# Optimization experiments

Hardware: AMD Instinct MI355X
Metric: run time of the kernel (lower is better)

The kernel has to match this reference:

```python
import jax, jax.numpy as jnp
import numpy as np

DIM = 512; LAYERS = 6; K = 15; VOCAB = 32000; B = 2; L = 1024
HID = 1024  # SwiGLU hidden: int(512*2) rounded up to multiple of 64
RANK = 64; BLOCK = 2048; MIX_W = 0.1
UP_DIL = [1, 2, 4, 8, 16, 32]
DN_DIL = UP_DIL[::-1]


def rmsnorm(x, w, eps=1e-6):
    return x * jax.lax.rsqrt(jnp.mean(x * x, axis=-1, keepdims=True) + eps) * w


def dconv(x, w, b, dil):
    # x: [B,D,T]; w: [D,1,K] depthwise; left (causal) padding of (K-1)*dil
    pad = (w.shape[-1] - 1) * dil
    y = jax.lax.conv_general_dilated(
        x, w, window_strides=(1,), padding=[(pad, 0)], rhs_dilation=(dil,),
        dimension_numbers=('NCH', 'OIH', 'NCH'), feature_group_count=x.shape[1])
    return y + b[None, :, None]


def conv_block(x, nw, cw, cb, w1, w2, w3, dil):
    # CausalDilatedConv: RMSNorm -> depthwise causal dilated conv -> silu -> SwiGLU -> +residual
    h = rmsnorm(x, nw)
    h = jax.nn.silu(dconv(jnp.transpose(h, (0, 2, 1)), cw, cb, dil))
    h = jnp.transpose(h, (0, 2, 1))
    h = jnp.einsum('bth,dh->btd',
                   jax.nn.silu(jnp.einsum('btd,hd->bth', h, w1)) * jnp.einsum('btd,hd->bth', h, w3),
                   w2)
    return h + x


def run_stack(x, dils, nw, cw, cb, w1, w2, w3, kp, ki, kd, gnorm):
    integral = x; previous = x; current = x
    for i, d in enumerate(dils):
        if i > 0:
            # PIDGate: step == i >= 1 so max(step,1) == i
            pid = kp[i-1] * current + ki[i-1] * (integral / i) + kd[i-1] * (current - previous)
            cur_in = rmsnorm(jax.nn.silu(pid), gnorm[i-1])
        else:
            cur_in = current
        current = conv_block(cur_in, nw[i], cw[i], cb[i], w1[i], w2[i], w3[i], d)
        previous = current
        integral = integral + current
    return current


def mix(x):
    # CausalMeanPool: x + 0.1 * causal running mean
    counts = jnp.arange(1, x.shape[1] + 1, dtype=x.dtype)[None, :, None]
    return x + MIX_W * jnp.cumsum(x, axis=1) / counts


def sgate(new, old, nw, dw, db, uw, ub):
    h = jax.nn.silu(rmsnorm(new, nw) @ dw.T + db)
    g = jax.nn.sigmoid(h @ uw.T + ub)
    return g * new + (1.0 - g) * old


def setup_inputs() -> dict:
    key = jax.random.key(0)
    ks = iter(jax.random.split(key, 64))
    def nrm(shape, s=0.02):
        return jax.random.normal(next(ks), shape, jnp.float32) * s
    def stack_params(p):
        return {
            p + '_norm_w': jnp.ones((LAYERS, DIM), jnp.float32),
            p + '_conv_w': nrm((LAYERS, DIM, 1, K), 0.1),
            p + '_conv_b': jnp.zeros((LAYERS, DIM), jnp.float32),
            p + '_w1': nrm((LAYERS, HID, DIM)),
            p + '_w2': nrm((LAYERS, DIM, HID)),
            p + '_w3': nrm((LAYERS, HID, DIM)),
            p + '_kp': jnp.full((LAYERS - 1, DIM), 0.5, jnp.float32),
            p + '_ki': jnp.full((LAYERS - 1, DIM), 0.3, jnp.float32),
            p + '_kd': jnp.full((LAYERS - 1, DIM), 0.2, jnp.float32),
            p + '_gnorm': jnp.ones((LAYERS - 1, DIM), jnp.float32),
        }
    inp = {
        'idx': jax.random.randint(next(ks), (B, L), 0, VOCAB),
        'emb': nrm((VOCAB, DIM)),
        'pos': nrm((1, BLOCK, DIM)),
        'emb_norm_w': jnp.ones((DIM,), jnp.float32),
        'token_shift': jnp.full((DIM,), 0.5, jnp.float32),
        'mem_gate_w': jnp.zeros((DIM, DIM), jnp.float32),  # nn.init.zeros_
        'mem_gate_b': nrm((DIM,)),
        'memory_p': jnp.zeros((B, DIM), jnp.float32),  # buffer, zero after reset()
        'sg_norm': jnp.ones((3, DIM), jnp.float32),
        'sg_down_w': nrm((3, RANK, DIM)),
        'sg_down_b': jnp.zeros((3, RANK), jnp.float32),
        'sg_up_w': nrm((3, DIM, RANK)),
        'sg_up_b': jnp.zeros((3, DIM), jnp.float32),
        'final_norm_w': jnp.ones((DIM,), jnp.float32),
    }
    inp.update(stack_params('up'))
    inp.update(stack_params('dn'))
    return inp


def _forward(idx, emb, pos, emb_norm_w, token_shift, mem_gate_w, mem_gate_b, memory_p,
             up_norm_w, up_conv_w, up_conv_b, up_w1, up_w2, up_w3, up_kp, up_ki, up_kd, up_gnorm,
             dn_norm_w, dn_conv_w, dn_conv_b, dn_w1, dn_w2, dn_w3, dn_kp, dn_ki, dn_kd, dn_gnorm,
             sg_norm, sg_down_w, sg_down_b, sg_up_w, sg_up_b, final_norm_w):
    T = idx.shape[1]
    x = emb[idx] + pos[:, :T]
    x = rmsnorm(x, emb_norm_w)
    # dropout is identity at eval time
    # memory injection: token-shift mix + sigmoid-gated persistent P-memory
    shifted = jnp.concatenate(
        [x[:, :1], token_shift * x[:, :-1] + (1.0 - token_shift) * x[:, 1:]], axis=1)
    mem = jax.nn.sigmoid(memory_p @ mem_gate_w.T + mem_gate_b)
    x = shifted + mem[:, None, :]
    initial = x
    up_p = (up_norm_w, up_conv_w, up_conv_b, up_w1, up_w2, up_w3, up_kp, up_ki, up_kd, up_gnorm)
    dn_p = (dn_norm_w, dn_conv_w, dn_conv_b, dn_w1, dn_w2, dn_w3, dn_kp, dn_ki, dn_kd, dn_gnorm)
    up1 = mix(run_stack(x, UP_DIL, *up_p))
    gated1 = sgate(up1, initial, sg_norm[0], sg_down_w[0], sg_down_b[0], sg_up_w[0], sg_up_b[0])
    down = mix(run_stack(gated1, DN_DIL, *dn_p))
    gated2 = sgate(down, initial, sg_norm[1], sg_down_w[1], sg_down_b[1], sg_up_w[1], sg_up_b[1])
    up2 = mix(run_stack(gated2, UP_DIL, *up_p))  # up_stack weights are shared/reused
    output = sgate(up2, gated2, sg_norm[2], sg_down_w[2], sg_down_b[2], sg_up_w[2], sg_up_b[2])
    output = rmsnorm(output, final_norm_w)
    return output @ emb.T  # tied head


def reference(idx, emb, pos, emb_norm_w, token_shift, mem_gate_w, mem_gate_b, memory_p,
              up_norm_w, up_conv_w, up_conv_b, up_w1, up_w2, up_w3, up_kp, up_ki, up_kd, up_gnorm,
              dn_norm_w, dn_conv_w, dn_conv_b, dn_w1, dn_w2, dn_w3, dn_kp, dn_ki, dn_kd, dn_gnorm,
              sg_norm, sg_down_w, sg_down_b, sg_up_w, sg_up_b, final_norm_w):
    return _forward(idx, emb, pos, emb_norm_w, token_shift, mem_gate_w, mem_gate_b, memory_p,
                    up_norm_w, up_conv_w, up_conv_b, up_w1, up_w2, up_w3, up_kp, up_ki, up_kd, up_gnorm,
                    dn_norm_w, dn_conv_w, dn_conv_b, dn_w1, dn_w2, dn_w3, dn_kp, dn_ki, dn_kd, dn_gnorm,
                    sg_norm, sg_down_w, sg_down_b, sg_up_w, sg_up_b, final_norm_w)
```

## Files before the change

### kernel.cpp

```cpp
#include <hip/hip_runtime.h>
#include <math.h>

#define DIM 512
#define NLAYERS 6
#define KSZ 15
#define VOCAB 32000
#define BATCH 2
#define SEQ 1024
#define HIDN 1024
#define RANK 64
#define NTOK (BATCH*SEQ)
#define MIXW 0.1f

typedef unsigned short u16;
typedef _Float16 f16;
typedef _Float16 f16x8 __attribute__((ext_vector_type(8)));
typedef _Float16 f16x4 __attribute__((ext_vector_type(4)));
typedef float  f32x4  __attribute__((ext_vector_type(4)));

__device__ __forceinline__ float sigm(float x){ return 1.f/(1.f+__expf(-x)); }

__device__ __forceinline__ float wred(float v){
  #pragma unroll
  for (int o=32;o>0;o>>=1) v += __shfl_xor(v, o, 64);
  return v;
}

#define MFMA16(a,b,c) __builtin_amdgcn_mfma_f32_16x16x32_f16(a,b,c,0,0,0)

__device__ __forceinline__ void gld16(const f16* g, f16* l){
  __builtin_amdgcn_global_load_lds(
      (const __attribute__((address_space(1))) void*)g,
      (__attribute__((address_space(3))) void*)l, 16, 0, 0);
}

__global__ __launch_bounds__(256) void k_cvt(const float* __restrict__ s,
    f16* __restrict__ d, long n4){
  long i = (long)blockIdx.x*256 + threadIdx.x;
  if (i >= n4) return;
  float4 v = reinterpret_cast<const float4*>(s)[i];
  f16x4 o; o.x=(f16)v.x; o.y=(f16)v.y; o.z=(f16)v.z; o.w=(f16)v.w;
  reinterpret_cast<f16x4*>(d)[i] = o;
}

__global__ __launch_bounds__(256) void k_cvtconv(const float* __restrict__ cw,
    float* __restrict__ cwT, int n){
  int i = blockIdx.x*256 + threadIdx.x;
  if (i >= n) return;
  int d = i & (DIM-1); int m = (i >> 9) % KSZ; int l = i / (KSZ*DIM);
  cwT[i] = cw[((size_t)l*DIM + d)*KSZ + (KSZ-1-m)];
}

__global__ __launch_bounds__(64) void k_embnorm(const int* __restrict__ idx,
    const float* __restrict__ emb, const float* __restrict__ pos,
    const float* __restrict__ w, float* __restrict__ out){
  int row = blockIdx.x;
  int t = row & (SEQ-1);
  int lane = threadIdx.x;
  long ebase = (long)idx[row]*DIM;
  long pbase = (long)t*DIM;
  float v[8]; float ss = 0.f;
  #pragma unroll
  for (int c=0;c<2;c++){
    int d = c*256 + lane*4;
    float4 e = *reinterpret_cast<const float4*>(emb + ebase + d);
    float4 p = *reinterpret_cast<const float4*>(pos + pbase + d);
    float x0 = e.x+p.x, x1 = e.y+p.y, x2 = e.z+p.z, x3 = e.w+p.w;
    v[c*4+0]=x0; v[c*4+1]=x1; v[c*4+2]=x2; v[c*4+3]=x3;
    ss += x0*x0 + x1*x1 + x2*x2 + x3*x3;
  }
  ss = wred(ss);
  float rs = rsqrtf(ss*(1.f/DIM) + 1e-6f);
  long ob = (long)row*DIM;
  #pragma unroll
  for (int c=0;c<2;c++){
    int d = c*256 + lane*4;
    float4 wv = *reinterpret_cast<const float4*>(w + d);
    float4 o;
    o.x = v[c*4+0]*rs*wv.x; o.y = v[c*4+1]*rs*wv.y;
    o.z = v[c*4+2]*rs*wv.z; o.w = v[c*4+3]*rs*wv.w;
    *reinterpret_cast<float4*>(out + ob + d) = o;
  }
}

__global__ void k_mem(const float* __restrict__ p, const float* __restrict__ gw,
                      const float* __restrict__ gb, float* __restrict__ mem){
  int i = blockIdx.x*blockDim.x + threadIdx.x;
  if (i >= BATCH*DIM) return;
  int b = i >> 9, d = i & (DIM-1);
  float acc = gb[d];
  const float* wr = gw + (long)d*DIM;
  const float* pr = p + b*DIM;
  for (int k=0;k<DIM;k+=4){
    float4 wv = *reinterpret_cast<const float4*>(wr+k);
    float4 pv = *reinterpret_cast<const float4*>(pr+k);
    acc += wv.x*pv.x + wv.y*pv.y + wv.z*pv.z + wv.w*pv.w;
  }
  mem[i] = sigm(acc);
}

__global__ void k_shift(const float* __restrict__ xn, const float* __restrict__ mem,
    const float* __restrict__ ts, float* __restrict__ out){
  int i = blockIdx.x*256 + threadIdx.x;
  int d = i & (DIM-1); int row = i >> 9; int t = row & (SEQ-1); int b = row >> 10;
  float cur = xn[i];
  float v;
  if (t == 0) v = cur;
  else { float f = ts[d]; v = f*xn[i-DIM] + (1.f-f)*cur; }
  out[i] = v + mem[b*DIM + d];
}

__global__ __launch_bounds__(64) void k_rms(const float* __restrict__ x,
    const float* __restrict__ w, f16* __restrict__ oh){
  int row = blockIdx.x; int lane = threadIdx.x;
  const float* xr = x + (long)row*DIM;
  float v[8]; float ss = 0.f;
  #pragma unroll
  for (int c=0;c<2;c++){
    int d = c*256 + lane*4;
    float4 f = *reinterpret_cast<const float4*>(xr + d);
    v[c*4+0]=f.x; v[c*4+1]=f.y; v[c*4+2]=f.z; v[c*4+3]=f.w;
    ss += f.x*f.x + f.y*f.y + f.z*f.z + f.w*f.w;
  }
  ss = wred(ss);
  float rs = rsqrtf(ss*(1.f/DIM) + 1e-6f);
  long ob = (long)row*DIM;
  #pragma unroll
  for (int c=0;c<2;c++){
    int d = c*256 + lane*4;
    float4 wv = *reinterpret_cast<const float4*>(w + d);
    f16x4 o;
    o.x = (f16)(v[c*4+0]*rs*wv.x); o.y = (f16)(v[c*4+1]*rs*wv.y);
    o.z = (f16)(v[c*4+2]*rs*wv.z); o.w = (f16)(v[c*4+3]*rs*wv.w);
    *reinterpret_cast<f16x4*>(oh + ob + d) = o;
  }
}

__global__ __launch_bounds__(64) void k_pid(const float* __restrict__ C,
    const float* __restrict__ I, float inv_i,
    const float* __restrict__ kp, const float* __restrict__ ki,
    const float* __restrict__ gn, const float* __restrict__ nw,
    float* __restrict__ xin, f16* __restrict__ oh){
  int row = blockIdx.x; int lane = threadIdx.x;
  long base = (long)row*DIM;
  float u[8]; float ss = 0.f;
  #pragma unroll
  for (int c=0;c<2;c++){
    int d = c*256 + lane*4;
    float4 cv = *reinterpret_cast<const float4*>(C + base + d);
    float4 iv = *reinterpret_cast<const float4*>(I + base + d);
    float4 kpv = *reinterpret_cast<const float4*>(kp + d);
    float4 kiv = *reinterpret_cast<const float4*>(ki + d);
    float p0 = kpv.x*cv.x + kiv.x*(iv.x*inv_i);
    float p1 = kpv.y*cv.y + kiv.y*(iv.y*inv_i);
    float p2 = kpv.z*cv.z + kiv.z*(iv.z*inv_i);
    float p3 = kpv.w*cv.w + kiv.w*(iv.w*inv_i);
    float s0 = p0*sigm(p0), s1 = p1*sigm(p1), s2 = p2*sigm(p2), s3 = p3*sigm(p3);
    u[c*4+0]=s0; u[c*4+1]=s1; u[c*4+2]=s2; u[c*4+3]=s3;
    ss += s0*s0 + s1*s1 + s2*s2 + s3*s3;
  }
  ss = wred(ss);
  float rs1 = rsqrtf(ss*(1.f/DIM) + 1e-6f);
  float x2[8]; float ss2 = 0.f;
  #pragma unroll
  for (int c=0;c<2;c++){
    int d = c*256 + lane*4;
    float4 gv = *reinterpret_cast<const float4*>(gn + d);
    float y0 = u[c*4+0]*rs1*gv.x, y1 = u[c*4+1]*rs1*gv.y;
    float y2 = u[c*4+2]*rs1*gv.z, y3 = u[c*4+3]*rs1*gv.w;
    x2[c*4+0]=y0; x2[c*4+1]=y1; x2[c*4+2]=y2; x2[c*4+3]=y3;
    ss2 += y0*y0 + y1*y1 + y2*y2 + y3*y3;
    float4 o; o.x=y0; o.y=y1; o.z=y2; o.w=y3;
    *reinterpret_cast<float4*>(xin + base + d) = o;
  }
  ss2 = wred(ss2);
  float rs2 = rsqrtf(ss2*(1.f/DIM) + 1e-6f);
  #pragma unroll
  for (int c=0;c<2;c++){
    int d = c*256 + lane*4;
    float4 nv = *reinterpret_cast<const float4*>(nw + d);
    f16x4 o;
    o.x = (f16)(x2[c*4+0]*rs2*nv.x); o.y = (f16)(x2[c*4+1]*rs2*nv.y);
    o.z = (f16)(x2[c*4+2]*rs2*nv.z); o.w = (f16)(x2[c*4+3]*rs2*nv.w);
    *reinterpret_cast<f16x4*>(oh + base + d) = o;
  }
}

__global__ __launch_bounds__(256) void k_conv(const f16* __restrict__ h1,
    const float* __restrict__ cwT, const float* __restrict__ cb,
    f16* __restrict__ hc, int dil){
  int i = blockIdx.x*256 + threadIdx.x;
  int d8 = (i & 63) << 3; int row = i >> 6; int t = row & (SEQ-1);
  float acc[8];
  {
    float4 b0 = *reinterpret_cast<const float4*>(&cb[d8]);
    float4 b1 = *reinterpret_cast<const float4*>(&cb[d8+4]);
    acc[0]=b0.x; acc[1]=b0.y; acc[2]=b0.z; acc[3]=b0.w;
    acc[4]=b1.x; acc[5]=b1.y; acc[6]=b1.z; acc[7]=b1.w;
  }
  #pragma unroll
  for (int m=0;m<KSZ;m++){
    if (t - m*dil >= 0){
      f16x8 h = *reinterpret_cast<const f16x8*>(&h1[(size_t)(row - m*dil)*DIM + d8]);
      float4 w0 = *reinterpret_cast<const float4*>(&cwT[m*DIM + d8]);
      float4 w1 = *reinterpret_cast<const float4*>(&cwT[m*DIM + d8 + 4]);
      acc[0]+=w0.x*(float)h[0]; acc[1]+=w0.y*(float)h[1];
      acc[2]+=w0.z*(float)h[2]; acc[3]+=w0.w*(float)h[3];
      acc[4]+=w1.x*(float)h[4]; acc[5]+=w1.y*(float)h[5];
      acc[6]+=w1.z*(float)h[6]; acc[7]+=w1.w*(float)h[7];
    }
  }
  f16x8 o;
  #pragma unroll
  for (int j=0;j<8;j++){ o[j] = (f16)(acc[j]*sigm(acc[j])); }
  *reinterpret_cast<f16x8*>(&hc[(size_t)row*DIM + d8]) = o;
}


__global__ __launch_bounds__(512) void k_dual(const f16* __restrict__ A,
    const f16* __restrict__ W1, const f16* __restrict__ W3, f16* __restrict__ G){
  __shared__ __align__(16) char smemc[50176];
  f16*   sB   = (f16*)smemc;
  float* stgf = (float*)smemc;
  float* kred = (float*)smemc + 4352;
  int tid = threadIdx.x, lane = tid&63, wid = tid>>6;
  int wk = wid>>2, wm = wid&3;
  int m0 = blockIdx.x*128, n0 = blockIdx.y*64;
  int r16 = lane&15, kq = lane>>4;

  auto stage = [&](int buf, int t){
    #pragma unroll
    for (int j=0;j<2;j++){
      int cc = j*512 + tid;
      int mat = cc>>9, c2 = cc&511, r = c2>>3, s = c2&7;
      const f16* src = (mat ? W3 : W1) + (size_t)(n0+r)*512 + t*64 + ((s^(r&7))<<3);
      gld16(src, sB + buf*8192 + (j*512 + wid*64)*8);
    }
  };

  f32x4 acc[2][4] = {};
  stage(0, 0);
  __syncthreads();
  #pragma unroll
  for (int t=0;t<8;t++){
    if (t < 7) stage((t&1)^1, t+1);
    f16x8 af[2][2];
    #pragma unroll
    for (int kk=0;kk<2;kk++)
      #pragma unroll
      for (int mf=0;mf<2;mf++){
        int row = m0 + wm*32 + mf*16 + r16;
        af[kk][mf] = *reinterpret_cast<const f16x8*>(A + (size_t)row*512 + t*64 + (kk*4+kq)*8);
      }
    const f16* sbt = sB + (t&1)*8192 + wk*4096;
    #pragma unroll
    for (int kk=0;kk<2;kk++){
      int kp0 = kk*4 + kq;
      f16x8 bf[4];
      #pragma unroll
      for (int nf=0;nf<4;nf++){
        int row = nf*16 + r16;
        bf[nf] = *reinterpret_cast<const f16x8*>(&sbt[row*64 + ((kp0^(row&7))<<3)]);
      }
      #pragma unroll
      for (int mf=0;mf<2;mf++)
        #pragma unroll
        for (int nf=0;nf<4;nf++)
          acc[mf][nf] = MFMA16(af[kk][mf], bf[nf], acc[mf][nf]);
    }
    __syncthreads();
  }
  if (wk == 1){
    #pragma unroll
    for (int mf=0;mf<2;mf++)
      #pragma unroll
      for (int nf=0;nf<4;nf++)
        *reinterpret_cast<f32x4*>(&kred[(((wm*2+mf)*4+nf)<<8) + lane*4]) = acc[mf][nf];
  }
  __syncthreads();
  if (wk == 1) return;
  int dr = (lane>>4)*4, dc = lane&15;
  float* stg = stgf + wm*1088;
  #pragma unroll
  for (int mf=0;mf<2;mf++){
    #pragma unroll
    for (int nf=0;nf<4;nf++){
      f32x4 a3 = *reinterpret_cast<f32x4*>(&kred[(((wm*2+mf)*4+nf)<<8) + lane*4]);
      #pragma unroll
      for (int q=0;q<4;q++){
        float x1 = acc[mf][nf][q];
        stg[(dr+q)*68 + nf*16 + dc] = x1*sigm(x1)*a3[q];
      }
    }
    int gmb = m0 + wm*32 + mf*16;
    #pragma unroll
    for (int pass=0;pass<2;pass++){
      int rr = pass*8 + (lane>>3), c = 8*(lane&7);
      float4 lo = *reinterpret_cast<float4*>(&stg[rr*68 + c]);
      float4 hi = *reinterpret_cast<float4*>(&stg[rr*68 + c + 4]);
      f16x8 o;
      o[0]=(f16)lo.x; o[1]=(f16)lo.y; o[2]=(f16)lo.z; o[3]=(f16)lo.w;
      o[4]=(f16)hi.x; o[5]=(f16)hi.y; o[6]=(f16)hi.z; o[7]=(f16)hi.w;
      *reinterpret_cast<f16x8*>(&G[(size_t)(gmb+rr)*HIDN + n0 + c]) = o;
    }
  }
}

__global__ __launch_bounds__(512) void k_w2(const f16* __restrict__ A,
    const f16* __restrict__ W, const float* __restrict__ XIN,
    float* __restrict__ OF, float* __restrict__ I, int init){
  __shared__ __align__(16) char smemc[33792];
  f16*   sB   = (f16*)smemc;
  float* stgf = (float*)smemc;
  float* kred = (float*)smemc + 4352;
  int tid = threadIdx.x, lane = tid&63, wid = tid>>6;
  int wk = wid>>2, wm = wid&3;
  int m0 = blockIdx.x*64, n0 = blockIdx.y*64;
  int r16 = lane&15, kq = lane>>4;

  auto stage = [&](int buf, int t){
    #pragma unroll
    for (int j=0;j<2;j++){
      int cc = j*512 + tid;
      int kg = cc>>9, c2 = cc&511, r = c2>>3, s = c2&7;
      const f16* src = W + (size_t)(n0+r)*1024 + kg*512 + t*64 + ((s^(r&7))<<3);
      gld16(src, sB + buf*8192 + (j*512 + wid*64)*8);
    }
  };

  f32x4 acc[4] = {};
  stage(0, 0);
  __syncthreads();
  #pragma unroll
  for (int t=0;t<8;t++){
    if (t < 7) stage((t&1)^1, t+1);
    f16x8 af[2];
    #pragma unroll
    for (int kk=0;kk<2;kk++){
      int row = m0 + wm*16 + r16;
      af[kk] = *reinterpret_cast<const f16x8*>(A + (size_t)row*1024 + wk*512 + t*64 + (kk*4+kq)*8);
    }
    const f16* sbt = sB + (t&1)*8192 + wk*4096;
    #pragma unroll
    for (int kk=0;kk<2;kk++){
      int kp0 = kk*4 + kq;
      #pragma unroll
      for (int nf=0;nf<4;nf++){
        int row = nf*16 + r16;
        f16x8 bf = *reinterpret_cast<const f16x8*>(&sbt[row*64 + ((kp0^(row&7))<<3)]);
        acc[nf] = MFMA16(af[kk], bf, acc[nf]);
      }
    }
    __syncthreads();
  }
  if (wk == 1){
    #pragma unroll
    for (int nf=0;nf<4;nf++)
      *reinterpret_cast<f32x4*>(&kred[((wm*4+nf)<<8) + lane*4]) = acc[nf];
  }
  __syncthreads();
  if (wk == 1) return;
  #pragma unroll
  for (int nf=0;nf<4;nf++){
    f32x4 p = *reinterpret_cast<f32x4*>(&kred[((wm*4+nf)<<8) + lane*4]);
    acc[nf][0]+=p[0]; acc[nf][1]+=p[1]; acc[nf][2]+=p[2]; acc[nf][3]+=p[3];
  }
  int dr = (lane>>4)*4, dc = lane&15;
  float* stg = stgf + wm*1088;
  #pragma unroll
  for (int nf=0;nf<4;nf++)
    #pragma unroll
    for (int q=0;q<4;q++)
      stg[(dr+q)*68 + nf*16 + dc] = acc[nf][q];
  int gmb = m0 + wm*16;
  #pragma unroll
  for (int pass=0;pass<4;pass++){
    int rr = pass*4 + (lane>>4), c = 4*(lane&15);
    float4 v = *reinterpret_cast<float4*>(&stg[rr*68 + c]);
    size_t o = (size_t)(gmb+rr)*DIM + n0 + c;
    float4 x = *reinterpret_cast<const float4*>(&XIN[o]);
    v.x+=x.x; v.y+=x.y; v.z+=x.z; v.w+=x.w;
    *reinterpret_cast<float4*>(&OF[o]) = v;
    float4 iv;
    if (init) iv = x;
    else      iv = *reinterpret_cast<const float4*>(&I[o]);
    iv.x+=v.x; iv.y+=v.y; iv.z+=v.z; iv.w+=v.w;
    *reinterpret_cast<float4*>(&I[o]) = iv;
  }
}

__global__ __launch_bounds__(512) void k_logits(const f16* __restrict__ A,
    const f16* __restrict__ E, float* __restrict__ OF){
  __shared__ __align__(16) char smemc[34816];
  f16*   sB   = (f16*)smemc;
  float* stgf = (float*)smemc;
  int tid = threadIdx.x, lane = tid&63, wid = tid>>6;
  int bid = blockIdx.x;
  int m0 = (bid&7)*256, n0 = (bid>>3)*64;
  int r16 = lane&15, kq = lane>>4;

  auto stage = [&](int buf, int t){
    int cc = tid;
    int r = cc>>3, s = cc&7;
    const f16* src = E + (size_t)(n0+r)*512 + t*64 + ((s^(r&7))<<3);
    gld16(src, sB + buf*4096 + wid*64*8);
  };

  f32x4 acc[2][4] = {};
  stage(0, 0);
  __syncthreads();
  #pragma unroll
  for (int t=0;t<8;t++){
    if (t < 7) stage((t&1)^1, t+1);
    f16x8 af[2][2];
    #pragma unroll
    for (int kk=0;kk<2;kk++)
      #pragma unroll
      for (int mf=0;mf<2;mf++){
        int row = m0 + wid*32 + mf*16 + r16;
        af[kk][mf] = *reinterpret_cast<const f16x8*>(A + (size_t)row*512 + t*64 + (kk*4+kq)*8);
      }
    const f16* sbt = sB + (t&1)*4096;
    #pragma unroll
    for (int kk=0;kk<2;kk++){
      int kp0 = kk*4 + kq;
      f16x8 bf[4];
      #pragma unroll
      for (int nf=0;nf<4;nf++){
        int row = nf*16 + r16;
        bf[nf] = *reinterpret_cast<const f16x8*>(&sbt[row*64 + ((kp0^(row&7))<<3)]);
      }
      #pragma unroll
      for (int mf=0;mf<2;mf++)
        #pragma unroll
        for (int nf=0;nf<4;nf++)
          acc[mf][nf] = MFMA16(af[kk][mf], bf[nf], acc[mf][nf]);
    }
    __syncthreads();
  }
  int dr = (lane>>4)*4, dc = lane&15;
  float* stg = stgf + wid*1088;
  #pragma unroll
  for (int mf=0;mf<2;mf++){
    #pragma unroll
    for (int nf=0;nf<4;nf++)
      #pragma unroll
      for (int q=0;q<4;q++)
        stg[(dr+q)*68 + nf*16 + dc] = acc[mf][nf][q];
    int gmb = m0 + wid*32 + mf*16;
    #pragma unroll
    for (int pass=0;pass<4;pass++){
      int rr = pass*4 + (lane>>4), c = 4*(lane&15);
      float4 v = *reinterpret_cast<float4*>(&stg[rr*68 + c]);
      *reinterpret_cast<float4*>(&OF[(size_t)(gmb+rr)*VOCAB + n0 + c]) = v;
    }
  }
}

__global__ __launch_bounds__(64) void k_mix(float* __restrict__ x){
  int col = blockIdx.x;
  int b = col >> 9, d = col & (DIM-1);
  int lane = threadIdx.x;
  long o = (long)b*SEQ*DIM + d + (long)lane*16*DIM;
  float v[16]; float s = 0.f;
  #pragma unroll
  for (int j=0;j<16;j++){ v[j] = x[o + (long)j*DIM]; s += v[j]; }
  float t = s;
  #pragma unroll
  for (int off=1; off<64; off<<=1){
    float u = __shfl_up(t, off, 64);
    if (lane >= off) t += u;
  }
  float run = t - s;
  #pragma unroll
  for (int j=0;j<16;j++){
    run += v[j];
    int tt = lane*16 + j;
    x[o + (long)j*DIM] = v[j] + MIXW*run/(float)(tt+1);
  }
}

__global__ __launch_bounds__(256) void k_sgate(const float* __restrict__ xnew,
    const float* __restrict__ xold, const float* __restrict__ nw,
    const float* __restrict__ dw, const float* __restrict__ db,
    const float* __restrict__ uw, const float* __restrict__ ub,
    float* __restrict__ out){
  __shared__ float raw[DIM];
  __shared__ float xn[DIM];
  __shared__ float part[256];
  __shared__ float hb[RANK];
  int row = blockIdx.x, tid = threadIdx.x;
  long base = (long)row*DIM;
  float ss = 0.f;
  for (int d=tid; d<DIM; d+=256){ float v = xnew[base+d]; raw[d]=v; ss += v*v; }
  ss = wred(ss);
  if ((tid&63)==0) part[tid>>6] = ss;
  __syncthreads();
  float tot = part[0]+part[1]+part[2]+part[3];
  float rs = rsqrtf(tot*(1.f/DIM)+1e-6f);
  for (int d=tid; d<DIM; d+=256) xn[d] = raw[d]*rs*nw[d];
  __syncthreads();
  int rr = tid & 63, q = tid >> 6;
  float p = 0.f;
  const float* dwr = dw + (long)rr*DIM + q*128;
  const float* xq = xn + q*128;
  #pragma unroll 8
  for (int d=0; d<128; d+=4){
    float4 wv = *reinterpret_cast<const float4*>(dwr+d);
    p += xq[d]*wv.x + xq[d+1]*wv.y + xq[d+2]*wv.z + xq[d+3]*wv.w;
  }
  part[tid] = p;
  __syncthreads();
  if (tid < RANK){
    float h = part[tid] + part[64+tid] + part[128+tid] + part[192+tid] + db[tid];
    hb[tid] = h * sigm(h);
  }
  __syncthreads();
  for (int d=tid; d<DIM; d+=256){
    float a = ub[d];
    const float* ur = uw + (long)d*RANK;
    #pragma unroll
    for (int rj=0;rj<RANK;rj+=4){
      float4 uv = *reinterpret_cast<const float4*>(ur+rj);
      a += hb[rj]*uv.x + hb[rj+1]*uv.y + hb[rj+2]*uv.z + hb[rj+3]*uv.w;
    }
    float g = sigm(a);
    out[base+d] = g*raw[d] + (1.f-g)*xold[base+d];
  }
}

extern "C" void kernel_launch(void* const* d_in, const int* in_sizes, int n_in,
                              void* d_out, int out_size, void* d_ws, size_t ws_size,
                              hipStream_t stream){
  const int*   idx           = (const int*)d_in[0];
  const float* emb           = (const float*)d_in[1];
  const float* pos           = (const float*)d_in[2];
  const float* emb_norm_w    = (const float*)d_in[3];
  const float* token_shift   = (const float*)d_in[4];
  const float* mem_gate_w    = (const float*)d_in[5];
  const float* mem_gate_b    = (const float*)d_in[6];
  const float* memory_p      = (const float*)d_in[7];
  const float* sg_norm       = (const float*)d_in[8];
  const float* sg_down_w     = (const float*)d_in[9];
  const float* sg_down_b     = (const float*)d_in[10];
  const float* sg_up_w       = (const float*)d_in[11];
  const float* sg_up_b       = (const float*)d_in[12];
  const float* final_norm_w  = (const float*)d_in[13];
  struct StackP { const float *nw, *cw, *cb, *w1, *w2, *w3, *kp, *ki, *gn; };
  StackP up { (const float*)d_in[14], (const float*)d_in[15], (const float*)d_in[16],
              (const float*)d_in[17], (const float*)d_in[18], (const float*)d_in[19],
              (const float*)d_in[20], (const float*)d_in[21], (const float*)d_in[23] };
  StackP dn { (const float*)d_in[24], (const float*)d_in[25], (const float*)d_in[26],
              (const float*)d_in[27], (const float*)d_in[28], (const float*)d_in[29],
              (const float*)d_in[30], (const float*)d_in[31], (const float*)d_in[33] };

  char* wp = (char*)d_ws;
  auto alloc = [&](size_t bytes)->void*{
    void* p = (void*)wp; wp += (bytes + 255) & ~(size_t)255; return p;
  };
  float* A0  = (float*)alloc((size_t)NTOK*DIM*4);
  float* A1  = (float*)alloc((size_t)NTOK*DIM*4);
  float* Cb  = (float*)alloc((size_t)NTOK*DIM*4);
  float* Ib  = (float*)alloc((size_t)NTOK*DIM*4);
  float* XIN = (float*)alloc((size_t)NTOK*DIM*4);
  f16*   H1  = (f16*)alloc((size_t)NTOK*DIM*2);
  f16*   HC  = (f16*)alloc((size_t)NTOK*DIM*2);
  f16*   G   = (f16*)alloc((size_t)NTOK*HIDN*2);
  const size_t WSZ = (size_t)NLAYERS*HIDN*DIM;
  f16*   UpW1 = (f16*)alloc(WSZ*2);
  f16*   UpW2 = (f16*)alloc(WSZ*2);
  f16*   UpW3 = (f16*)alloc(WSZ*2);
  f16*   DnW1 = (f16*)alloc(WSZ*2);
  f16*   DnW2 = (f16*)alloc(WSZ*2);
  f16*   DnW3 = (f16*)alloc(WSZ*2);
  f16*   Ef   = (f16*)alloc((size_t)VOCAB*DIM*2);
  float* UpCT = (float*)alloc((size_t)NLAYERS*KSZ*DIM*4);
  float* DnCT = (float*)alloc((size_t)NLAYERS*KSZ*DIM*4);
  float* MEM  = (float*)alloc((size_t)BATCH*DIM*4);

  static const int updil[NLAYERS] = {1,2,4,8,16,32};
  static const int dndil[NLAYERS] = {32,16,8,4,2,1};

  {
    long n4 = WSZ/4;
    int g = (int)((n4 + 255)/256);
    k_cvt<<<g,256,0,stream>>>(up.w1, UpW1, n4);
    k_cvt<<<g,256,0,stream>>>(up.w2, UpW2, n4);
    k_cvt<<<g,256,0,stream>>>(up.w3, UpW3, n4);
    k_cvt<<<g,256,0,stream>>>(dn.w1, DnW1, n4);
    k_cvt<<<g,256,0,stream>>>(dn.w2, DnW2, n4);
    k_cvt<<<g,256,0,stream>>>(dn.w3, DnW3, n4);
    long e4 = (long)VOCAB*DIM/4;
    k_cvt<<<(int)((e4+255)/256),256,0,stream>>>(emb, Ef, e4);
    int nc = NLAYERS*KSZ*DIM;
    k_cvtconv<<<(nc+255)/256,256,0,stream>>>(up.cw, UpCT, nc);
    k_cvtconv<<<(nc+255)/256,256,0,stream>>>(dn.cw, DnCT, nc);
  }

  k_embnorm<<<NTOK,64,0,stream>>>(idx, emb, pos, emb_norm_w, Cb);
  k_mem<<<(BATCH*DIM+255)/256,256,0,stream>>>(memory_p, mem_gate_w, mem_gate_b, MEM);
  k_shift<<<NTOK*DIM/256,256,0,stream>>>(Cb, MEM, token_shift, A0);

  auto run_stack = [&](const float* xs, const StackP& S, const float* CT,
                       const f16* W1f, const f16* W2f, const f16* W3f, const int* dil){
    for (int l=0;l<NLAYERS;l++){
      const float* bin;
      if (l==0){
        bin = xs;
        k_rms<<<NTOK,64,0,stream>>>(xs, S.nw + l*DIM, H1);
      } else {
        k_pid<<<NTOK,64,0,stream>>>(Cb, Ib, 1.f/(float)l,
            S.kp+(l-1)*DIM, S.ki+(l-1)*DIM, S.gn+(l-1)*DIM, S.nw+l*DIM, XIN, H1);
        bin = XIN;
      }
      k_conv<<<NTOK*DIM/8/256,256,0,stream>>>(H1, CT + (size_t)l*KSZ*DIM, S.cb + l*DIM, HC, dil[l]);
      k_dual<<<dim3(NTOK/128, HIDN/64),512,0,stream>>>(
          HC, W1f + (size_t)l*HIDN*DIM, W3f + (size_t)l*HIDN*DIM, G);
      k_w2<<<dim3(NTOK/64, DIM/64),512,0,stream>>>(
          G, W2f + (size_t)l*DIM*HIDN, bin, Cb, Ib, (l==0)?1:0);
    }
  };

  run_stack(A0, up, UpCT, UpW1, UpW2, UpW3, updil);
  k_mix<<<BATCH*DIM,64,0,stream>>>(Cb);
  k_sgate<<<NTOK,256,0,stream>>>(Cb, A0, sg_norm, sg_down_w, sg_down_b, sg_up_w, sg_up_b, A1);
  run_stack(A1, dn, DnCT, DnW1, DnW2, DnW3, dndil);
  k_mix<<<BATCH*DIM,64,0,stream>>>(Cb);
  k_sgate<<<NTOK,256,0,stream>>>(Cb, A0, sg_norm+DIM, sg_down_w+RANK*DIM, sg_down_b+RANK,
                                 sg_up_w+DIM*RANK, sg_up_b+DIM, A1);
  run_stack(A1, up, UpCT, UpW1, UpW2, UpW3, updil);
  k_mix<<<BATCH*DIM,64,0,stream>>>(Cb);
  k_sgate<<<NTOK,256,0,stream>>>(Cb, A1, sg_norm+2*DIM, sg_down_w+2*RANK*DIM, sg_down_b+2*RANK,
                                 sg_up_w+2*DIM*RANK, sg_up_b+2*DIM, Cb);
  k_rms<<<NTOK,64,0,stream>>>(Cb, final_norm_w, H1);
  k_logits<<<8*(VOCAB/64),512,0,stream>>>(H1, Ef, (float*)d_out);
}
```

Measured before the change: 1.222 ms.

## Use 4-stage async LDS pipeline in GEMM kernels, drop split-K

Rewrites k_dual, k_w2 and k_logits to use a four-buffer global_load_lds pipeline that stays three stages ahead, with explicit vmcnt waits and a single barrier per step in place of double buffering with two syncs. k_dual and k_w2 drop the intra-block split-K across two wave groups and the LDS reduction. They now use 256-thread blocks with smaller M/N tiles, so more blocks are launched. k_dual computes W1 and W3 products in the same wave from one A fragment. The vmcnt counts are hand-tuned to the per-stage load count and are fragile if the load pattern changes.

```diff
diff --git a/kernel.cpp b/kernel.cpp
--- a/kernel.cpp
+++ b/kernel.cpp
@@ -32,6 +32,14 @@
   __builtin_amdgcn_global_load_lds(
       (const __attribute__((address_space(1))) void*)g,
       (__attribute__((address_space(3))) void*)l, 16, 0, 0);
+}
+
+template<int N> __device__ __forceinline__ void vwait(){
+  asm volatile("s_waitcnt vmcnt(%0)" :: "i"(N) : "memory");
+}
+__device__ __forceinline__ void pipe_bar(){
+  __builtin_amdgcn_s_barrier();
+  __builtin_amdgcn_sched_barrier(0);
 }
 
 __global__ __launch_bounds__(256) void k_cvt(const float* __restrict__ s,
@@ -217,166 +225,119 @@
 }
 
 
-__global__ __launch_bounds__(512) void k_dual(const f16* __restrict__ A,
+__global__ __launch_bounds__(256) void k_dual(const f16* __restrict__ A,
     const f16* __restrict__ W1, const f16* __restrict__ W3, f16* __restrict__ G){
-  __shared__ __align__(16) char smemc[50176];
-  f16*   sB   = (f16*)smemc;
-  float* stgf = (float*)smemc;
-  float* kred = (float*)smemc + 4352;
+  __shared__ __align__(16) f16 smem[4*8192];
   int tid = threadIdx.x, lane = tid&63, wid = tid>>6;
-  int wk = wid>>2, wm = wid&3;
-  int m0 = blockIdx.x*128, n0 = blockIdx.y*64;
+  int m0 = blockIdx.x*64, n0 = blockIdx.y*64;
   int r16 = lane&15, kq = lane>>4;
 
   auto stage = [&](int buf, int t){
     #pragma unroll
-    for (int j=0;j<2;j++){
-      int cc = j*512 + tid;
+    for (int j=0;j<4;j++){
+      int cc = j*256 + tid;
       int mat = cc>>9, c2 = cc&511, r = c2>>3, s = c2&7;
       const f16* src = (mat ? W3 : W1) + (size_t)(n0+r)*512 + t*64 + ((s^(r&7))<<3);
-      gld16(src, sB + buf*8192 + (j*512 + wid*64)*8);
-    }
-  };
-
-  f32x4 acc[2][4] = {};
-  stage(0, 0);
-  __syncthreads();
-  #pragma unroll
-  for (int t=0;t<8;t++){
-    if (t < 7) stage((t&1)^1, t+1);
-    f16x8 af[2][2];
-    #pragma unroll
-    for (int kk=0;kk<2;kk++)
-      #pragma unroll
-      for (int mf=0;mf<2;mf++){
-        int row = m0 + wm*32 + mf*16 + r16;
-        af[kk][mf] = *reinterpret_cast<const f16x8*>(A + (size_t)row*512 + t*64 + (kk*4+kq)*8);
-      }
-    const f16* sbt = sB + (t&1)*8192 + wk*4096;
+      gld16(src, smem + buf*8192 + (j*256 + wid*64)*8);
+    }
+  };
+  f32x4 a1[4] = {}, a3[4] = {};
+  auto compute = [&](int t){
+    const f16* sbt = smem + (t&3)*8192;
     #pragma unroll
     for (int kk=0;kk<2;kk++){
       int kp0 = kk*4 + kq;
-      f16x8 bf[4];
+      f16x8 av = *reinterpret_cast<const f16x8*>(
+          A + (size_t)(m0 + wid*16 + r16)*512 + t*64 + kp0*8);
       #pragma unroll
       for (int nf=0;nf<4;nf++){
         int row = nf*16 + r16;
-        bf[nf] = *reinterpret_cast<const f16x8*>(&sbt[row*64 + ((kp0^(row&7))<<3)]);
+        f16x8 b1 = *reinterpret_cast<const f16x8*>(&sbt[row*64 + ((kp0^(row&7))<<3)]);
+        f16x8 b3 = *reinterpret_cast<const f16x8*>(&sbt[4096 + row*64 + ((kp0^(row&7))<<3)]);
+        a1[nf] = MFMA16(av, b1, a1[nf]);
+        a3[nf] = MFMA16(av, b3, a3[nf]);
       }
-      #pragma unroll
-      for (int mf=0;mf<2;mf++)
-        #pragma unroll
-        for (int nf=0;nf<4;nf++)
-          acc[mf][nf] = MFMA16(af[kk][mf], bf[nf], acc[mf][nf]);
-    }
-    __syncthreads();
-  }
-  if (wk == 1){
-    #pragma unroll
-    for (int mf=0;mf<2;mf++)
-      #pragma unroll
-      for (int nf=0;nf<4;nf++)
-        *reinterpret_cast<f32x4*>(&kred[(((wm*2+mf)*4+nf)<<8) + lane*4]) = acc[mf][nf];
-  }
-  __syncthreads();
-  if (wk == 1) return;
+    }
+  };
+  stage(0,0); stage(1,1); stage(2,2);
+#define DITER(T,NW) { vwait<NW>(); pipe_bar(); if ((T)+3 < 8) stage(((T)+3)&3,(T)+3); compute(T); }
+  DITER(0,8) DITER(1,8) DITER(2,8) DITER(3,8) DITER(4,8) DITER(5,8) DITER(6,4) DITER(7,0)
+#undef DITER
+  __syncthreads();
+  float* stg = (float*)smem + wid*1088;
   int dr = (lane>>4)*4, dc = lane&15;
-  float* stg = stgf + wm*1088;
-  #pragma unroll
-  for (int mf=0;mf<2;mf++){
-    #pragma unroll
-    for (int nf=0;nf<4;nf++){
-      f32x4 a3 = *reinterpret_cast<f32x4*>(&kred[(((wm*2+mf)*4+nf)<<8) + lane*4]);
-      #pragma unroll
-      for (int q=0;q<4;q++){
-        float x1 = acc[mf][nf][q];
-        stg[(dr+q)*68 + nf*16 + dc] = x1*sigm(x1)*a3[q];
-      }
-    }
-    int gmb = m0 + wm*32 + mf*16;
-    #pragma unroll
-    for (int pass=0;pass<2;pass++){
-      int rr = pass*8 + (lane>>3), c = 8*(lane&7);
-      float4 lo = *reinterpret_cast<float4*>(&stg[rr*68 + c]);
-      float4 hi = *reinterpret_cast<float4*>(&stg[rr*68 + c + 4]);
-      f16x8 o;
-      o[0]=(f16)lo.x; o[1]=(f16)lo.y; o[2]=(f16)lo.z; o[3]=(f16)lo.w;
-      o[4]=(f16)hi.x; o[5]=(f16)hi.y; o[6]=(f16)hi.z; o[7]=(f16)hi.w;
-      *reinterpret_cast<f16x8*>(&G[(size_t)(gmb+rr)*HIDN + n0 + c]) = o;
-    }
-  }
-}
-
-__global__ __launch_bounds__(512) void k_w2(const f16* __restrict__ A,
+  #pragma unroll
+  for (int nf=0;nf<4;nf++)
+    #pragma unroll
+    for (int q=0;q<4;q++){
+      float x1 = a1[nf][q];
+      stg[(dr+q)*68 + nf*16 + dc] = x1*sigm(x1)*a3[nf][q];
+    }
+  int gmb = m0 + wid*16;
+  #pragma unroll
+  for (int pass=0;pass<2;pass++){
+    int rr = pass*8 + (lane>>3), c = 8*(lane&7);
+    float4 lo = *reinterpret_cast<float4*>(&stg[rr*68 + c]);
+    float4 hi = *reinterpret_cast<float4*>(&stg[rr*68 + c + 4]);
+    f16x8 o;
+    o[0]=(f16)lo.x; o[1]=(f16)lo.y; o[2]=(f16)lo.z; o[3]=(f16)lo.w;
+    o[4]=(f16)hi.x; o[5]=(f16)hi.y; o[6]=(f16)hi.z; o[7]=(f16)hi.w;
+    *reinterpret_cast<f16x8*>(&G[(size_t)(gmb+rr)*HIDN + n0 + c]) = o;
+  }
+}
+
+__global__ __launch_bounds__(256) void k_w2(const f16* __restrict__ A,
     const f16* __restrict__ W, const float* __restrict__ XIN,
     float* __restrict__ OF, float* __restrict__ I, int init){
-  __shared__ __align__(16) char smemc[33792];
-  f16*   sB   = (f16*)smemc;
-  float* stgf = (float*)smemc;
-  float* kred = (float*)smemc + 4352;
+  __shared__ __align__(16) f16 smem[4*4096];
   int tid = threadIdx.x, lane = tid&63, wid = tid>>6;
-  int wk = wid>>2, wm = wid&3;
-  int m0 = blockIdx.x*64, n0 = blockIdx.y*64;
+  int m0 = blockIdx.x*64, n0 = blockIdx.y*32;
   int r16 = lane&15, kq = lane>>4;
 
   auto stage = [&](int buf, int t){
     #pragma unroll
     for (int j=0;j<2;j++){
-      int cc = j*512 + tid;
-      int kg = cc>>9, c2 = cc&511, r = c2>>3, s = c2&7;
-      const f16* src = W + (size_t)(n0+r)*1024 + kg*512 + t*64 + ((s^(r&7))<<3);
-      gld16(src, sB + buf*8192 + (j*512 + wid*64)*8);
-    }
-  };
-
-  f32x4 acc[4] = {};
-  stage(0, 0);
-  __syncthreads();
-  #pragma unroll
-  for (int t=0;t<8;t++){
-    if (t < 7) stage((t&1)^1, t+1);
-    f16x8 af[2];
-    #pragma unroll
-    for (int kk=0;kk<2;kk++){
-      int row = m0 + wm*16 + r16;
-      af[kk] = *reinterpret_cast<const f16x8*>(A + (size_t)row*1024 + wk*512 + t*64 + (kk*4+kq)*8);
-    }
-    const f16* sbt = sB + (t&1)*8192 + wk*4096;
-    #pragma unroll
-    for (int kk=0;kk<2;kk++){
+      int cc = j*256 + tid;
+      int r = cc>>4, s = cc&15;
+      int g = (s&8) | ((s^(r&7))&7);
+      const f16* src = W + (size_t)(n0+r)*1024 + t*128 + (g<<3);
+      gld16(src, smem + buf*4096 + (j*256 + wid*64)*8);
+    }
+  };
+  f32x4 acc[2] = {};
+  auto compute = [&](int t){
+    const f16* sbt = smem + (t&3)*4096;
+    #pragma unroll
+    for (int kk=0;kk<4;kk++){
       int kp0 = kk*4 + kq;
+      f16x8 av = *reinterpret_cast<const f16x8*>(
+          A + (size_t)(m0 + wid*16 + r16)*1024 + t*128 + kp0*8);
       #pragma unroll
-      for (int nf=0;nf<4;nf++){
+      for (int nf=0;nf<2;nf++){
         int row = nf*16 + r16;
-        f16x8 bf = *reinterpret_cast<const f16x8*>(&sbt[row*64 + ((kp0^(row&7))<<3)]);
-        acc[nf] = MFMA16(af[kk], bf, acc[nf]);
+        int sl = (kp0&8) | ((kp0^(row&7))&7);
+        f16x8 bv = *reinterpret_cast<const f16x8*>(&sbt[row*128 + (sl<<3)]);
+        acc[nf] = MFMA16(av, bv, acc[nf]);
       }
     }
-    __syncthreads();
-  }
-  if (wk == 1){
-    #pragma unroll
-    for (int nf=0;nf<4;nf++)
-      *reinterpret_cast<f32x4*>(&kred[((wm*4+nf)<<8) + lane*4]) = acc[nf];
-  }
-  __syncthreads();
-  if (wk == 1) return;
-  #pragma unroll
-  for (int nf=0;nf<4;nf++){
-    f32x4 p = *reinterpret_cast<f32x4*>(&kred[((wm*4+nf)<<8) + lane*4]);
-    acc[nf][0]+=p[0]; acc[nf][1]+=p[1]; acc[nf][2]+=p[2]; acc[nf][3]+=p[3];
-  }
+  };
+  stage(0,0); stage(1,1); stage(2,2);
+#define WITER(T,NW) { vwait<NW>(); pipe_bar(); if ((T)+3 < 8) stage(((T)+3)&3,(T)+3); compute(T); }
+  WITER(0,4) WITER(1,4) WITER(2,4) WITER(3,4) WITER(4,4) WITER(5,4) WITER(6,2) WITER(7,0)
+#undef WITER
+  __syncthreads();
+  float* stg = (float*)smem + wid*(16*36);
   int dr = (lane>>4)*4, dc = lane&15;
-  float* stg = stgf + wm*1088;
-  #pragma unroll
-  for (int nf=0;nf<4;nf++)
+  #pragma unroll
+  for (int nf=0;nf<2;nf++)
     #pragma unroll
     for (int q=0;q<4;q++)
-      stg[(dr+q)*68 + nf*16 + dc] = acc[nf][q];
-  int gmb = m0 + wm*16;
-  #pragma unroll
-  for (int pass=0;pass<4;pass++){
-    int rr = pass*4 + (lane>>4), c = 4*(lane&15);
-    float4 v = *reinterpret_cast<float4*>(&stg[rr*68 + c]);
+      stg[(dr+q)*36 + nf*16 + dc] = acc[nf][q];
+  int gmb = m0 + wid*16;
+  #pragma unroll
+  for (int pass=0;pass<2;pass++){
+    int rr = pass*8 + (lane>>3), c = 4*(lane&7);
+    float4 v = *reinterpret_cast<float4*>(&stg[rr*36 + c]);
     size_t o = (size_t)(gmb+rr)*DIM + n0 + c;
     float4 x = *reinterpret_cast<const float4*>(&XIN[o]);
     v.x+=x.x; v.y+=x.y; v.z+=x.z; v.w+=x.w;
@@ -392,8 +353,7 @@
 __global__ __launch_bounds__(512) void k_logits(const f16* __restrict__ A,
     const f16* __restrict__ E, float* __restrict__ OF){
   __shared__ __align__(16) char smemc[34816];
-  f16*   sB   = (f16*)smemc;
-  float* stgf = (float*)smemc;
+  f16* sB = (f16*)smemc;
   int tid = threadIdx.x, lane = tid&63, wid = tid>>6;
   int bid = blockIdx.x;
   int m0 = (bid&7)*256, n0 = (bid>>3)*64;
@@ -402,44 +362,36 @@
   auto stage = [&](int buf, int t){
     int cc = tid;
     int r = cc>>3, s = cc&7;
-    const f16* src = E + (size_t)(n0+r)*512 + t*64 + ((s^(r&7))<<3);
-    gld16(src, sB + buf*4096 + wid*64*8);
-  };
-
+    gld16(E + (size_t)(n0+r)*512 + t*64 + ((s^(r&7))<<3), sB + buf*4096 + wid*64*8);
+  };
   f32x4 acc[2][4] = {};
-  stage(0, 0);
-  __syncthreads();
-  #pragma unroll
-  for (int t=0;t<8;t++){
-    if (t < 7) stage((t&1)^1, t+1);
-    f16x8 af[2][2];
-    #pragma unroll
-    for (int kk=0;kk<2;kk++)
-      #pragma unroll
-      for (int mf=0;mf<2;mf++){
-        int row = m0 + wid*32 + mf*16 + r16;
-        af[kk][mf] = *reinterpret_cast<const f16x8*>(A + (size_t)row*512 + t*64 + (kk*4+kq)*8);
-      }
-    const f16* sbt = sB + (t&1)*4096;
+  auto compute = [&](int t){
+    const f16* sbt = sB + (t&3)*4096;
     #pragma unroll
     for (int kk=0;kk<2;kk++){
       int kp0 = kk*4 + kq;
-      f16x8 bf[4];
+      f16x8 af[2];
+      #pragma unroll
+      for (int mf=0;mf<2;mf++)
+        af[mf] = *reinterpret_cast<const f16x8*>(
+            A + (size_t)(m0 + wid*32 + mf*16 + r16)*512 + t*64 + kp0*8);
       #pragma unroll
       for (int nf=0;nf<4;nf++){
         int row = nf*16 + r16;
-        bf[nf] = *reinterpret_cast<const f16x8*>(&sbt[row*64 + ((kp0^(row&7))<<3)]);
+        f16x8 bv = *reinterpret_cast<const f16x8*>(&sbt[row*64 + ((kp0^(row&7))<<3)]);
+        #pragma unroll
+        for (int mf=0;mf<2;mf++)
+          acc[mf][nf] = MFMA16(af[mf], bv, acc[mf][nf]);
       }
-      #pragma unroll
-      for (int mf=0;mf<2;mf++)
-        #pragma unroll
-        for (int nf=0;nf<4;nf++)
-          acc[mf][nf] = MFMA16(af[kk][mf], bf[nf], acc[mf][nf]);
-    }
-    __syncthreads();
-  }
+    }
+  };
+  stage(0,0); stage(1,1); stage(2,2);
+#define LITER(T,NW) { vwait<NW>(); pipe_bar(); if ((T)+3 < 8) stage(((T)+3)&3,(T)+3); compute(T); }
+  LITER(0,2) LITER(1,2) LITER(2,2) LITER(3,2) LITER(4,2) LITER(5,2) LITER(6,1) LITER(7,0)
+#undef LITER
+  __syncthreads();
   int dr = (lane>>4)*4, dc = lane&15;
-  float* stg = stgf + wid*1088;
+  float* stg = (float*)smemc + wid*1088;
   #pragma unroll
   for (int mf=0;mf<2;mf++){
     #pragma unroll
@@ -614,9 +566,9 @@
         bin = XIN;
       }
       k_conv<<<NTOK*DIM/8/256,256,0,stream>>>(H1, CT + (size_t)l*KSZ*DIM, S.cb + l*DIM, HC, dil[l]);
-      k_dual<<<dim3(NTOK/128, HIDN/64),512,0,stream>>>(
+      k_dual<<<dim3(NTOK/64, HIDN/64),256,0,stream>>>(
           HC, W1f + (size_t)l*HIDN*DIM, W3f + (size_t)l*HIDN*DIM, G);
-      k_w2<<<dim3(NTOK/64, DIM/64),512,0,stream>>>(
+      k_w2<<<dim3(NTOK/64, DIM/32),256,0,stream>>>(
           G, W2f + (size_t)l*DIM*HIDN, bin, Cb, Ib, (l==0)?1:0);
     }
   };
```

Measured after the change: 1.164 ms. -4.8%, faster.
